# Performance work log

Hardware: AMD Instinct MI355X
Metric: run time of the kernel (lower is better)

Reference implementation:

```python
import jax, jax.numpy as jnp
import numpy as np
import math

HEADS = 8
DIM_KEY = 64
WINDOW = 128
DIM = 512
NUM_REL_POS_FEATURES = 512  # = HEADS*DIM_KEY; %4==0 and %6!=0 -> exp + central_mask features
W_WIDTH, W_FRAC = 8, 4
X_WIDTH, X_FRAC = 8, 4


def quantize(x, width, frac_width):
    # MASE integer_quantizer: fixed-point round+clamp (STE in bwd, identity here).
    scale = 2.0 ** frac_width
    lo = -(2.0 ** (width - 1))
    hi = 2.0 ** (width - 1) - 1.0
    q = jnp.clip(jnp.round(x * scale), lo, hi) / scale
    return x + jax.lax.stop_gradient(q - x)


def get_positional_embed(window, feature_size):
    # distances in [-(W-1), W-1]
    d = jnp.arange(-(window - 1), window, dtype=jnp.float32)  # [2W-1]
    nb = feature_size // 4  # 2 feature fns * 2 components
    ad = jnp.abs(d)[:, None]
    # exponential features
    max_range = math.log(window) / math.log(2.0)
    half_life = 2.0 ** jnp.linspace(3.0, max_range, nb)
    e = jnp.exp(-math.log(2.0) / half_life[None, :] * ad)  # [2W-1, nb]
    # central mask features (2**128 overflows to inf in f32, matching torch)
    cw = 2.0 ** jnp.arange(1, nb + 1, dtype=jnp.float32) - 1.0
    c = (cw[None, :] > ad).astype(jnp.float32)  # [2W-1, nb]
    emb = jnp.concatenate([e, c], axis=-1)  # [2W-1, 2*nb]
    return jnp.concatenate([emb, jnp.sign(d)[:, None] * emb], axis=-1)  # [2W-1, 4*nb]


def relative_shift_swin(x):
    # x: [b, h, w, t1, t2] with t2 = 2*t1 - 1 -> [b, h, w, t1, t1]
    b, h, w, t1, t2 = x.shape
    x = jnp.concatenate([jnp.zeros_like(x[..., :1]), x], axis=-1)  # pad -> t2+1 = 2*t1
    t2p = t2 + 1
    x = x.reshape(b, h, w, t2p, t1)[:, :, :, 1:, :]
    x = x.reshape(b, h, w, t1, t2p - 1)
    return x[..., :(t2p + 1) // 2]


def setup_inputs() -> dict:
    key = jax.random.key(0)
    ks = jax.random.split(key, 7)
    b, n = 4, 8192
    hd = HEADS * DIM_KEY
    return {
        "x": jax.random.normal(ks[0], (b, n, DIM), dtype=jnp.float32),
        "w_qkv": jax.random.normal(ks[1], (hd * 3, DIM), dtype=jnp.float32) * 0.02,
        "w_out": jax.random.normal(ks[2], (DIM, hd), dtype=jnp.float32) * 0.02,
        "b_out": jnp.zeros((DIM,), dtype=jnp.float32),
        "w_rel": jax.random.normal(ks[3], (hd, NUM_REL_POS_FEATURES), dtype=jnp.float32) * 0.02,
        "rel_content_bias": jax.random.normal(ks[4], (1, HEADS, 1, 1, DIM_KEY), dtype=jnp.float32),
        "rel_pos_bias": jax.random.normal(ks[5], (1, HEADS, 1, 1, DIM_KEY), dtype=jnp.float32),
    }


def reference(x, w_qkv, w_out, b_out, w_rel, rel_content_bias, rel_pos_bias):
    b, n, c = x.shape
    w = n // WINDOW  # n divisible by window -> no padding path
    xq = quantize(x, X_WIDTH, X_FRAC)
    wq = quantize(w_qkv, W_WIDTH, W_FRAC)
    wo = quantize(w_out, W_WIDTH, W_FRAC)

    qkv = xq @ wq.T  # [b, n, 3*h*d], last dim laid out as (h, d, k)
    qkv = qkv.reshape(b, n, HEADS, DIM_KEY, 3)
    q = qkv[..., 0].transpose(0, 2, 1, 3)  # [b, h, n, d]
    k = qkv[..., 1].transpose(0, 2, 1, 3)
    v = qkv[..., 2].transpose(0, 2, 1, 3)

    qw = q.reshape(b, HEADS, w, WINDOW, DIM_KEY)
    kw = k.reshape(b, HEADS, w, WINDOW, DIM_KEY)
    vw = v.reshape(b, HEADS, w, WINDOW, DIM_KEY)

    positions = get_positional_embed(WINDOW, NUM_REL_POS_FEATURES)  # [2W-1, F]
    rel_k = positions @ w_rel.T  # [2W-1, h*d]  (rel_pos_embedding weight is NOT quantized)
    rel_k = rel_k.reshape(2 * WINDOW - 1, HEADS, DIM_KEY).transpose(1, 0, 2)  # [h, 2W-1, d]

    scale = DIM_KEY ** -0.5
    content_attn = jnp.einsum('bhwqd,bhwkd->bhwqk', qw + rel_content_bias, kw) * scale
    # NB: positional logits are intentionally unscaled, as in the source.
    rel_logits = jnp.einsum('bhwqd,hkd->bhwqk', qw + rel_pos_bias, rel_k)  # [b,h,w,W,2W-1]
    position_attn = relative_shift_swin(rel_logits)  # [b,h,w,W,W]

    attn = jax.nn.softmax(content_attn + position_attn, axis=-1)
    out = jnp.einsum('bhwqk,bhwkd->bhwqd', attn, vw)  # [b,h,w,W,d]
    out = out.transpose(0, 2, 3, 1, 4).reshape(b, w, WINDOW, HEADS * DIM_KEY)
    out = out @ wo.T + b_out  # [b, w, W, dim]
    return out.reshape(b, n, -1)
```

## Files before the change

kernel.cpp:

```cpp
#include <hip/hip_runtime.h>

typedef unsigned short u16;
typedef unsigned int u32;
typedef __attribute__((ext_vector_type(8))) __bf16 bf16x8;
typedef __attribute__((ext_vector_type(4))) float f32x4;
typedef __attribute__((ext_vector_type(8))) unsigned short u16x8;
typedef __attribute__((ext_vector_type(4))) unsigned short u16x4;

#define GLL(gp, lp) __builtin_amdgcn_global_load_lds((const __attribute__((address_space(1))) void*)(gp), (__attribute__((address_space(3))) void*)(lp), 16, 0, 0)

__device__ __forceinline__ u16 f2bf(float f) {
  u32 u = __float_as_uint(f);
  u += 0x7FFFu + ((u >> 16) & 1u);
  return (u16)(u >> 16);
}
__device__ __forceinline__ float bf2f(u16 u) { return __uint_as_float(((u32)u) << 16); }
__device__ __forceinline__ float qz(float v) {
  float r = rintf(v * 16.0f);
  r = fminf(127.0f, fmaxf(-128.0f, r));
  return r * 0.0625f;
}
__device__ __forceinline__ f32x4 mfma16(bf16x8 a, bf16x8 b, f32x4 c) {
  return __builtin_amdgcn_mfma_f32_16x16x32_bf16(a, b, c, 0, 0, 0);
}

__global__ __launch_bounds__(256) void k_quant(const float* __restrict__ x,
                                               const float* __restrict__ wqkv,
                                               const float* __restrict__ wout,
                                               u16* __restrict__ xq,
                                               u16* __restrict__ wq,
                                               u16* __restrict__ wo) {
  const int X4 = 4194304;
  const int W4 = 196608;
  const int O4 = 65536;
  int stride = gridDim.x * blockDim.x;
  for (int i = blockIdx.x * blockDim.x + threadIdx.x; i < X4 + W4 + O4; i += stride) {
    const float4* s; u16* d; int jl, jd;
    if (i < X4) {
      s = (const float4*)x; d = xq; jl = i; jd = i;
    } else if (i < X4 + W4) {
      s = (const float4*)wqkv; d = wq;
      jl = i - X4;
      int rs = jl >> 7;
      int jc = jl & 127;
      int h = rs / 192;
      int rem = rs - h * 192;
      int dd = rem / 3;
      int comp = rem - dd * 3;
      jd = (comp * 512 + h * 64 + dd) * 128 + jc;
    } else {
      s = (const float4*)wout; d = wo; jl = i - X4 - W4; jd = jl;
    }
    float4 v = s[jl];
    u16x4 o;
    o.x = f2bf(qz(v.x)); o.y = f2bf(qz(v.y)); o.z = f2bf(qz(v.z)); o.w = f2bf(qz(v.w));
    *(u16x4*)(d + (size_t)jd * 4) = o;
  }
}

__global__ __launch_bounds__(128) void k_relk(const float* __restrict__ w_rel,
                                              const float* __restrict__ pb,
                                              u16* __restrict__ relk,
                                              float* __restrict__ pbR) {
  int r = blockIdx.x;
  int cseg = blockIdx.y;
  int tid = threadIdx.x;
  int c = cseg * 128 + tid;
  if (r == 255) {
    relk[((size_t)(c >> 6) * 256 + 255) * 64 + (c & 63)] = 0;
    if ((tid & 63) == 0) pbR[(c >> 6) * 256 + 255] = 0.f;
    return;
  }
  __shared__ float pos[512];
  float dd = (float)(r - 127);
  float ad = fabsf(dd);
  float sg = (dd > 0.f) ? 1.f : ((dd < 0.f) ? -1.f : 0.f);
  for (int f = tid; f < 512; f += 128) {
    int base = f & 255;
    float feat;
    if (base < 128) {
      float hl = exp2f(3.0f + (float)base * (4.0f / 127.0f));
      feat = expf((-0.6931471805599453f / hl) * ad);
    } else {
      float cw = exp2f((float)(base - 128 + 1)) - 1.0f;
      feat = (cw > ad) ? 1.0f : 0.0f;
    }
    if (f >= 256) feat *= sg;
    pos[f] = feat;
  }
  __syncthreads();
  const float4* wr4 = (const float4*)(w_rel + (size_t)c * 512);
  float acc = 0.f;
  #pragma unroll 4
  for (int f4 = 0; f4 < 128; f4++) {
    float4 w4 = wr4[f4];
    int f = f4 * 4;
    acc += pos[f] * w4.x + pos[f + 1] * w4.y + pos[f + 2] * w4.z + pos[f + 3] * w4.w;
  }
  relk[((size_t)(c >> 6) * 256 + r) * 64 + (c & 63)] = f2bf(acc);
  float contrib = acc * pb[c];
  #pragma unroll
  for (int off = 1; off < 64; off <<= 1) contrib += __shfl_xor(contrib, off, 64);
  if ((tid & 63) == 0) pbR[(c >> 6) * 256 + r] = contrib;
}

__global__ __launch_bounds__(256) void k_gemm_qkv(const u16* __restrict__ Aq,
                                                  const u16* __restrict__ Bq,
                                                  u16* __restrict__ Qo,
                                                  u16* __restrict__ Ko,
                                                  u16* __restrict__ Vo) {
  __shared__ u16 As[128 * 32];
  __shared__ u16 Bs[128 * 32];
  int tid = threadIdx.x;
  int bid = blockIdx.x;
  int swz = (bid & 7) * (gridDim.x >> 3) + (bid >> 3);
  int m0 = (swz / 12) * 128, n0 = (swz % 12) * 128;
  int wid = tid >> 6, lane = tid & 63, g = lane >> 4, r16 = lane & 15;
  int wm = wid >> 1, wn = wid & 1;
  f32x4 acc[4][4];
  #pragma unroll
  for (int i = 0; i < 4; i++)
    #pragma unroll
    for (int j = 0; j < 4; j++) acc[i][j] = (f32x4){0.f, 0.f, 0.f, 0.f};
  const u16* Ab = Aq + (size_t)m0 * 512;
  const u16* Bb = Bq + (size_t)n0 * 512;
  char* AsB = (char*)As + wid * 1024;
  char* BsB = (char*)Bs + wid * 1024;
  int srow = tid >> 2;
  int scol = ((tid & 3) ^ ((tid >> 3) & 3)) * 8;
  int gs = (g ^ ((r16 >> 1) & 3)) * 8;
  for (int k0 = 0; k0 < 512; k0 += 32) {
    __syncthreads();
    GLL(Ab + (size_t)srow * 512 + k0 + scol, AsB);
    GLL(Ab + (size_t)(srow + 64) * 512 + k0 + scol, AsB + 4096);
    GLL(Bb + (size_t)srow * 512 + k0 + scol, BsB);
    GLL(Bb + (size_t)(srow + 64) * 512 + k0 + scol, BsB + 4096);
    __syncthreads();
    bf16x8 a[4], b[4];
    #pragma unroll
    for (int mt = 0; mt < 4; mt++)
      a[mt] = *(const bf16x8*)(As + (wm * 64 + mt * 16 + r16) * 32 + gs);
    #pragma unroll
    for (int nt = 0; nt < 4; nt++)
      b[nt] = *(const bf16x8*)(Bs + (wn * 64 + nt * 16 + r16) * 32 + gs);
    #pragma unroll
    for (int mt = 0; mt < 4; mt++)
      #pragma unroll
      for (int nt = 0; nt < 4; nt++) acc[mt][nt] = mfma16(a[mt], b[nt], acc[mt][nt]);
  }
  #pragma unroll
  for (int nt = 0; nt < 4; nt++) {
    int colc = n0 + wn * 64 + nt * 16 + r16;
    int comp = colc >> 9;
    int hd = colc & 511;
    u16* dst = (comp == 0) ? Qo : (comp == 1 ? Ko : Vo);
    u16* dstp = dst + (size_t)(hd >> 6) * 524288 + (hd & 63);
    #pragma unroll
    for (int mt = 0; mt < 4; mt++) {
      int mbase = m0 + wm * 64 + mt * 16 + 4 * g;
      #pragma unroll
      for (int rr = 0; rr < 4; rr++) {
        int m = mbase + rr;
        int bb = m >> 13, nn = m & 8191;
        dstp[(size_t)bb * 4194304 + (size_t)nn * 64] = f2bf(acc[mt][nt][rr]);
      }
    }
  }
}

__global__ __launch_bounds__(512) void k_attn(const u16* __restrict__ Q,
                                              const u16* __restrict__ K,
                                              const u16* __restrict__ V,
                                              const u16* __restrict__ relk,
                                              const float* __restrict__ pbR,
                                              const float* __restrict__ cb,
                                              u16* __restrict__ attout) {
  int bid = blockIdx.x;
  int bb = bid >> 9;
  int h = (bid >> 6) & 7;
  int w = bid & 63;
  int tid = threadIdx.x;
  int s = tid >> 6;
  int lane = tid & 63, g = lane >> 4, r16 = lane & 15;
  const int n0 = w * 128;
  const u16* Qh = Q + ((size_t)(bb * 8 + h) * 8192 + n0) * 64;
  const u16* Kh = K + ((size_t)(bb * 8 + h) * 8192 + n0) * 64;
  const u16* Vh = V + ((size_t)(bb * 8 + h) * 8192 + n0) * 64;
  const u16* Rh = relk + (size_t)h * 256 * 64;
  const float* pbRh = pbR + h * 256;

  __shared__ u16 VT[64 * 128];
  __shared__ u16 Pst[8 * 16 * 128];
  __shared__ float cbK[128];

  {
    int rv = tid >> 2, c0 = (tid & 3) << 4;
    const u16* src = Vh + rv * 64 + c0;
    u16x8 v0 = *(const u16x8*)src;
    u16x8 v1 = *(const u16x8*)(src + 8);
    int chunk = rv >> 3, sub = rv & 7;
    #pragma unroll
    for (int j = 0; j < 8; j++) {
      int dv = c0 + j;
      VT[dv * 128 + ((chunk ^ (dv & 7)) << 3) + sub] = v0[j];
    }
    #pragma unroll
    for (int j = 0; j < 8; j++) {
      int dv = c0 + 8 + j;
      VT[dv * 128 + ((chunk ^ (dv & 7)) << 3) + sub] = v1[j];
    }
  }
  if (tid < 128) {
    const u16x8* kr8 = (const u16x8*)(Kh + tid * 64);
    const float* cbh = cb + h * 64;
    float a = 0.f;
    #pragma unroll
    for (int d8 = 0; d8 < 8; d8++) {
      u16x8 kv = kr8[d8];
      #pragma unroll
      for (int j = 0; j < 8; j++) a += cbh[d8 * 8 + j] * bf2f(kv[j]);
    }
    cbK[tid] = a;
  }

  const u16* qptr = Qh + ((s << 4) + r16) * 64 + (g << 3);
  bf16x8 qa0 = *(const bf16x8*)qptr;
  bf16x8 qa1 = *(const bf16x8*)(qptr + 32);

  f32x4 sc[8];
  #pragma unroll
  for (int kt = 0; kt < 8; kt++) {
    const u16* kp = Kh + ((kt << 4) + r16) * 64 + (g << 3);
    bf16x8 b0 = *(const bf16x8*)kp;
    bf16x8 b1 = *(const bf16x8*)(kp + 32);
    f32x4 c = {0.f, 0.f, 0.f, 0.f};
    c = mfma16(qa0, b0, c);
    sc[kt] = mfma16(qa1, b1, c);
  }
  f32x4 rl[9];
  #pragma unroll
  for (int t = 0; t < 9; t++) {
    int ct = 7 - s + t;
    const u16* rp = Rh + ((ct << 4) + r16) * 64 + (g << 3);
    bf16x8 b0 = *(const bf16x8*)rp;
    bf16x8 b1 = *(const bf16x8*)(rp + 32);
    f32x4 c = {0.f, 0.f, 0.f, 0.f};
    c = mfma16(qa0, b0, c);
    c = mfma16(qa1, b1, c);
    float pv = pbRh[(ct << 4) + r16];
    c[0] += pv; c[1] += pv; c[2] += pv; c[3] += pv;
    rl[t] = c;
  }
  __syncthreads();

  #pragma unroll
  for (int kt = 0; kt < 8; kt++) {
    float cbk = cbK[(kt << 4) + r16];
    #pragma unroll
    for (int rr = 0; rr < 4; rr++) {
      int qq = 4 * g + rr;
      int loc = 15 + r16 - qq;
      int srcl = (g << 4) | (loc & 15);
      float vlo = __shfl(rl[kt][rr], srcl, 64);
      float vhi = __shfl(rl[kt + 1][rr], srcl, 64);
      float pos = (loc < 16) ? vlo : vhi;
      sc[kt][rr] = (sc[kt][rr] + cbk) * 0.125f + pos;
    }
  }
  float inv[4];
  #pragma unroll
  for (int rr = 0; rr < 4; rr++) {
    float m = sc[0][rr];
    #pragma unroll
    for (int kt = 1; kt < 8; kt++) m = fmaxf(m, sc[kt][rr]);
    #pragma unroll
    for (int off = 1; off < 16; off <<= 1) m = fmaxf(m, __shfl_xor(m, off, 64));
    float sum = 0.f;
    #pragma unroll
    for (int kt = 0; kt < 8; kt++) {
      float p = expf(sc[kt][rr] - m);
      sc[kt][rr] = p;
      sum += p;
    }
    #pragma unroll
    for (int off = 1; off < 16; off <<= 1) sum += __shfl_xor(sum, off, 64);
    inv[rr] = 1.0f / sum;
  }
  u16* Pw = Pst + s * (16 * 128);
  #pragma unroll
  for (int kt = 0; kt < 8; kt++) {
    #pragma unroll
    for (int rr = 0; rr < 4; rr++) {
      int qq = 4 * g + rr;
      int k = (kt << 4) + r16;
      Pw[qq * 128 + ((((k >> 3)) ^ (qq & 7)) << 3) + (k & 7)] = f2bf(sc[kt][rr]);
    }
  }
  f32x4 o[4];
  #pragma unroll
  for (int dvt = 0; dvt < 4; dvt++) o[dvt] = (f32x4){0.f, 0.f, 0.f, 0.f};
  #pragma unroll
  for (int koff = 0; koff < 128; koff += 32) {
    int ach = (koff >> 3) + g;
    bf16x8 a = *(const bf16x8*)(Pw + r16 * 128 + ((ach ^ (r16 & 7)) << 3));
    #pragma unroll
    for (int dvt = 0; dvt < 4; dvt++) {
      int dv = dvt * 16 + r16;
      bf16x8 bv = *(const bf16x8*)(VT + dv * 128 + ((ach ^ (dv & 7)) << 3));
      o[dvt] = mfma16(a, bv, o[dvt]);
    }
  }
  #pragma unroll
  for (int dvt = 0; dvt < 4; dvt++) {
    #pragma unroll
    for (int rr = 0; rr < 4; rr++) {
      int qq = 4 * g + rr;
      int nrow = n0 + (s << 4) + qq;
      int colo = h * 64 + dvt * 16 + r16;
      attout[((size_t)bb * 8192 + nrow) * 512 + colo] = f2bf(o[dvt][rr] * inv[rr]);
    }
  }
}

__global__ __launch_bounds__(256) void k_gemm_out(const u16* __restrict__ Aq,
                                                  const u16* __restrict__ Bq,
                                                  const float* __restrict__ bias,
                                                  float* __restrict__ out) {
  __shared__ u16 As[128 * 32];
  __shared__ u16 Bs[128 * 32];
  int tid = threadIdx.x;
  int bid = blockIdx.x;
  int swz = (bid & 7) * (gridDim.x >> 3) + (bid >> 3);
  int m0 = (swz >> 2) * 128, n0 = (swz & 3) * 128;
  int wid = tid >> 6, lane = tid & 63, g = lane >> 4, r16 = lane & 15;
  int wm = wid >> 1, wn = wid & 1;
  f32x4 acc[4][4];
  #pragma unroll
  for (int i = 0; i < 4; i++)
    #pragma unroll
    for (int j = 0; j < 4; j++) acc[i][j] = (f32x4){0.f, 0.f, 0.f, 0.f};
  const u16* Ab = Aq + (size_t)m0 * 512;
  const u16* Bb = Bq + (size_t)n0 * 512;
  char* AsB = (char*)As + wid * 1024;
  char* BsB = (char*)Bs + wid * 1024;
  int srow = tid >> 2;
  int scol = ((tid & 3) ^ ((tid >> 3) & 3)) * 8;
  int gs = (g ^ ((r16 >> 1) & 3)) * 8;
  for (int k0 = 0; k0 < 512; k0 += 32) {
    __syncthreads();
    GLL(Ab + (size_t)srow * 512 + k0 + scol, AsB);
    GLL(Ab + (size_t)(srow + 64) * 512 + k0 + scol, AsB + 4096);
    GLL(Bb + (size_t)srow * 512 + k0 + scol, BsB);
    GLL(Bb + (size_t)(srow + 64) * 512 + k0 + scol, BsB + 4096);
    __syncthreads();
    bf16x8 a[4], b[4];
    #pragma unroll
    for (int mt = 0; mt < 4; mt++)
      a[mt] = *(const bf16x8*)(As + (wm * 64 + mt * 16 + r16) * 32 + gs);
    #pragma unroll
    for (int nt = 0; nt < 4; nt++)
      b[nt] = *(const bf16x8*)(Bs + (wn * 64 + nt * 16 + r16) * 32 + gs);
    #pragma unroll
    for (int mt = 0; mt < 4; mt++)
      #pragma unroll
      for (int nt = 0; nt < 4; nt++) acc[mt][nt] = mfma16(a[mt], b[nt], acc[mt][nt]);
  }
  #pragma unroll
  for (int nt = 0; nt < 4; nt++) {
    int col = n0 + wn * 64 + nt * 16 + r16;
    float bv = bias[col];
    #pragma unroll
    for (int mt = 0; mt < 4; mt++) {
      int mbase = m0 + wm * 64 + mt * 16 + 4 * g;
      #pragma unroll
      for (int rr = 0; rr < 4; rr++) {
        int m = mbase + rr;
        out[(size_t)m * 512 + col] = acc[mt][nt][rr] + bv;
      }
    }
  }
}

extern "C" void kernel_launch(void* const* d_in, const int* in_sizes, int n_in,
                              void* d_out, int out_size, void* d_ws, size_t ws_size,
                              hipStream_t stream) {
  const float* x     = (const float*)d_in[0];
  const float* w_qkv = (const float*)d_in[1];
  const float* w_out = (const float*)d_in[2];
  const float* b_out = (const float*)d_in[3];
  const float* w_rel = (const float*)d_in[4];
  const float* cb    = (const float*)d_in[5];
  const float* pb    = (const float*)d_in[6];
  float* out = (float*)d_out;

  char* p = (char*)d_ws;
  u16* xq   = (u16*)p; p += (size_t)32768 * 512 * 2;
  u16* wq   = (u16*)p; p += (size_t)1536 * 512 * 2;
  u16* wo   = (u16*)p; p += (size_t)512 * 512 * 2;
  u16* relk = (u16*)p; p += (size_t)8 * 256 * 64 * 2;
  float* pbR = (float*)p; p += (size_t)8 * 256 * 4;
  u16* Qb   = (u16*)p; p += (size_t)4 * 8 * 8192 * 64 * 2;
  u16* Kb   = (u16*)p; p += (size_t)4 * 8 * 8192 * 64 * 2;
  u16* Vb   = (u16*)p; p += (size_t)4 * 8 * 8192 * 64 * 2;
  u16* att  = (u16*)p; p += (size_t)32768 * 512 * 2;

  hipLaunchKernelGGL(k_quant, dim3(2048), dim3(256), 0, stream, x, w_qkv, w_out, xq, wq, wo);
  hipLaunchKernelGGL(k_relk, dim3(256, 4), dim3(128), 0, stream, w_rel, pb, relk, pbR);
  hipLaunchKernelGGL(k_gemm_qkv, dim3(3072), dim3(256), 0, stream, xq, wq, Qb, Kb, Vb);
  hipLaunchKernelGGL(k_attn, dim3(2048), dim3(512), 0, stream, Qb, Kb, Vb, relk, pbR, cb, att);
  hipLaunchKernelGGL(k_gemm_out, dim3(1024), dim3(256), 0, stream, att, wo, b_out, out);
}
```

Before: 359.5 us.

## Transpose attention MFMA operands to keep P in registers and drop LDS staging

Swaps the MFMA operand order so each lane owns one query row's scores. The P matrix can then be passed to the PV MFMA through cross-lane shuffles instead of being staged through LDS. Relative-position tiles are now computed inside the score loop and realigned with register rotations plus a single shuffle pair, which lowers register pressure. Softmax reductions need only two xor-shuffles, and outputs are written as packed bf16 pairs. The V transpose uses 32-bit LDS writes, and the launch bounds request higher occupancy, at the cost of extra shuffle work and more intricate lane-index logic.

```diff
diff --git a/kernel.cpp b/kernel.cpp
--- a/kernel.cpp
+++ b/kernel.cpp
@@ -6,6 +6,7 @@
 typedef __attribute__((ext_vector_type(4))) float f32x4;
 typedef __attribute__((ext_vector_type(8))) unsigned short u16x8;
 typedef __attribute__((ext_vector_type(4))) unsigned short u16x4;
+typedef __attribute__((ext_vector_type(4))) unsigned int u32x4;
 
 #define GLL(gp, lp) __builtin_amdgcn_global_load_lds((const __attribute__((address_space(1))) void*)(gp), (__attribute__((address_space(3))) void*)(lp), 16, 0, 0)
 
@@ -15,6 +16,11 @@
   return (u16)(u >> 16);
 }
 __device__ __forceinline__ float bf2f(u16 u) { return __uint_as_float(((u32)u) << 16); }
+__device__ __forceinline__ u32 cvtpk(float lo, float hi) {
+  u32 r;
+  asm("v_cvt_pk_bf16_f32 %0, %1, %2" : "=v"(r) : "v"(lo), "v"(hi));
+  return r;
+}
 __device__ __forceinline__ float qz(float v) {
   float r = rintf(v * 16.0f);
   r = fminf(127.0f, fmaxf(-128.0f, r));
@@ -168,13 +174,28 @@
   }
 }
 
-__global__ __launch_bounds__(512) void k_attn(const u16* __restrict__ Q,
-                                              const u16* __restrict__ K,
-                                              const u16* __restrict__ V,
-                                              const u16* __restrict__ relk,
-                                              const float* __restrict__ pbR,
-                                              const float* __restrict__ cb,
-                                              u16* __restrict__ attout) {
+__device__ __forceinline__ f32x4 rel_tile(const u16* __restrict__ Rh,
+                                          const float* __restrict__ pbRh,
+                                          bf16x8 qb0, bf16x8 qb1,
+                                          int ct, int r16, int g) {
+  const u16* rp = Rh + ((ct << 4) + r16) * 64 + (g << 3);
+  bf16x8 rb0 = *(const bf16x8*)rp;
+  bf16x8 rb1 = *(const bf16x8*)(rp + 32);
+  f32x4 c = {0.f, 0.f, 0.f, 0.f};
+  c = mfma16(rb0, qb0, c);
+  c = mfma16(rb1, qb1, c);
+  f32x4 pv = *(const f32x4*)(pbRh + (ct << 4) + (g << 2));
+  c[0] += pv[0]; c[1] += pv[1]; c[2] += pv[2]; c[3] += pv[3];
+  return c;
+}
+
+__global__ __launch_bounds__(512, 8) void k_attn(const u16* __restrict__ Q,
+                                                 const u16* __restrict__ K,
+                                                 const u16* __restrict__ V,
+                                                 const u16* __restrict__ relk,
+                                                 const float* __restrict__ pbR,
+                                                 const float* __restrict__ cb,
+                                                 u16* __restrict__ attout) {
   int bid = blockIdx.x;
   int bb = bid >> 9;
   int h = (bid >> 6) & 7;
@@ -190,24 +211,22 @@
   const float* pbRh = pbR + h * 256;
 
   __shared__ u16 VT[64 * 128];
-  __shared__ u16 Pst[8 * 16 * 128];
   __shared__ float cbK[128];
 
   {
-    int rv = tid >> 2, c0 = (tid & 3) << 4;
-    const u16* src = Vh + rv * 64 + c0;
+    int r2 = tid >> 3;
+    int c0 = (tid & 7) << 3;
+    const u16* src = Vh + r2 * 128 + c0;
     u16x8 v0 = *(const u16x8*)src;
-    u16x8 v1 = *(const u16x8*)(src + 8);
-    int chunk = rv >> 3, sub = rv & 7;
+    u16x8 v1 = *(const u16x8*)(src + 64);
+    int kc = r2 >> 2;
+    int pos = (r2 & 3) << 1;
     #pragma unroll
     for (int j = 0; j < 8; j++) {
       int dv = c0 + j;
-      VT[dv * 128 + ((chunk ^ (dv & 7)) << 3) + sub] = v0[j];
-    }
-    #pragma unroll
-    for (int j = 0; j < 8; j++) {
-      int dv = c0 + 8 + j;
-      VT[dv * 128 + ((chunk ^ (dv & 7)) << 3) + sub] = v1[j];
+      int swzv = (dv ^ (dv >> 3)) & 7;
+      u32 wv = (u32)v0[j] | ((u32)v1[j] << 16);
+      *(u32*)(VT + dv * 128 + ((kc ^ swzv) << 3) + pos) = wv;
     }
   }
   if (tid < 128) {
@@ -224,100 +243,124 @@
   }
 
   const u16* qptr = Qh + ((s << 4) + r16) * 64 + (g << 3);
-  bf16x8 qa0 = *(const bf16x8*)qptr;
-  bf16x8 qa1 = *(const bf16x8*)(qptr + 32);
+  bf16x8 qb0 = *(const bf16x8*)qptr;
+  bf16x8 qb1 = *(const bf16x8*)(qptr + 32);
 
   f32x4 sc[8];
   #pragma unroll
   for (int kt = 0; kt < 8; kt++) {
     const u16* kp = Kh + ((kt << 4) + r16) * 64 + (g << 3);
-    bf16x8 b0 = *(const bf16x8*)kp;
-    bf16x8 b1 = *(const bf16x8*)(kp + 32);
+    bf16x8 kf0 = *(const bf16x8*)kp;
+    bf16x8 kf1 = *(const bf16x8*)(kp + 32);
     f32x4 c = {0.f, 0.f, 0.f, 0.f};
-    c = mfma16(qa0, b0, c);
-    sc[kt] = mfma16(qa1, b1, c);
-  }
-  f32x4 rl[9];
-  #pragma unroll
-  for (int t = 0; t < 9; t++) {
-    int ct = 7 - s + t;
-    const u16* rp = Rh + ((ct << 4) + r16) * 64 + (g << 3);
-    bf16x8 b0 = *(const bf16x8*)rp;
-    bf16x8 b1 = *(const bf16x8*)(rp + 32);
-    f32x4 c = {0.f, 0.f, 0.f, 0.f};
-    c = mfma16(qa0, b0, c);
-    c = mfma16(qa1, b1, c);
-    float pv = pbRh[(ct << 4) + r16];
-    c[0] += pv; c[1] += pv; c[2] += pv; c[3] += pv;
-    rl[t] = c;
-  }
+    c = mfma16(kf0, qb0, c);
+    sc[kt] = mfma16(kf1, qb1, c);
+  }
+
+  int a0 = (3 - r16) & 3;
+  bool rb0s = (a0 & 1) != 0, rb1s = (a0 & 2) != 0;
+  float rotA[4], rotB[4];
+  {
+    f32x4 rl = rel_tile(Rh, pbRh, qb0, qb1, 7 - s, r16, g);
+    float s1[4];
+    #pragma unroll
+    for (int i = 0; i < 4; i++) s1[i] = rb0s ? rl[(i + 1) & 3] : rl[i];
+    #pragma unroll
+    for (int i = 0; i < 4; i++) rotA[i] = rb1s ? s1[(i + 2) & 3] : s1[i];
+  }
+  int srcl[4]; bool hisel[4];
+  #pragma unroll
+  for (int rr = 0; rr < 4; rr++) {
+    int loc = 15 + 4 * g + rr - r16;
+    srcl[rr] = (((loc & 15) >> 2) << 4) | r16;
+    hisel[rr] = loc >= 16;
+  }
+
   __syncthreads();
 
   #pragma unroll
   for (int kt = 0; kt < 8; kt++) {
-    float cbk = cbK[(kt << 4) + r16];
+    f32x4 rl = rel_tile(Rh, pbRh, qb0, qb1, 8 - s + kt, r16, g);
+    float s1[4];
+    #pragma unroll
+    for (int i = 0; i < 4; i++) s1[i] = rb0s ? rl[(i + 1) & 3] : rl[i];
+    #pragma unroll
+    for (int i = 0; i < 4; i++) rotB[i] = rb1s ? s1[(i + 2) & 3] : s1[i];
+    f32x4 cbv = *(const f32x4*)(&cbK[(kt << 4) + (g << 2)]);
     #pragma unroll
     for (int rr = 0; rr < 4; rr++) {
-      int qq = 4 * g + rr;
-      int loc = 15 + r16 - qq;
-      int srcl = (g << 4) | (loc & 15);
-      float vlo = __shfl(rl[kt][rr], srcl, 64);
-      float vhi = __shfl(rl[kt + 1][rr], srcl, 64);
-      float pos = (loc < 16) ? vlo : vhi;
-      sc[kt][rr] = (sc[kt][rr] + cbk) * 0.125f + pos;
-    }
-  }
-  float inv[4];
-  #pragma unroll
-  for (int rr = 0; rr < 4; rr++) {
-    float m = sc[0][rr];
-    #pragma unroll
-    for (int kt = 1; kt < 8; kt++) m = fmaxf(m, sc[kt][rr]);
-    #pragma unroll
-    for (int off = 1; off < 16; off <<= 1) m = fmaxf(m, __shfl_xor(m, off, 64));
-    float sum = 0.f;
-    #pragma unroll
-    for (int kt = 0; kt < 8; kt++) {
-      float p = expf(sc[kt][rr] - m);
+      float vlo = __shfl(rotA[rr], srcl[rr], 64);
+      float vhi = __shfl(rotB[rr], srcl[rr], 64);
+      float posv = hisel[rr] ? vhi : vlo;
+      sc[kt][rr] = (sc[kt][rr] + cbv[rr]) * 0.125f + posv;
+    }
+    #pragma unroll
+    for (int i = 0; i < 4; i++) rotA[i] = rotB[i];
+  }
+
+  float mx = sc[0][0];
+  #pragma unroll
+  for (int kt = 0; kt < 8; kt++)
+    #pragma unroll
+    for (int rr = 0; rr < 4; rr++) mx = fmaxf(mx, sc[kt][rr]);
+  mx = fmaxf(mx, __shfl_xor(mx, 16, 64));
+  mx = fmaxf(mx, __shfl_xor(mx, 32, 64));
+  float sum = 0.f;
+  #pragma unroll
+  for (int kt = 0; kt < 8; kt++)
+    #pragma unroll
+    for (int rr = 0; rr < 4; rr++) {
+      float p = expf(sc[kt][rr] - mx);
       sc[kt][rr] = p;
       sum += p;
     }
-    #pragma unroll
-    for (int off = 1; off < 16; off <<= 1) sum += __shfl_xor(sum, off, 64);
-    inv[rr] = 1.0f / sum;
-  }
-  u16* Pw = Pst + s * (16 * 128);
+  sum += __shfl_xor(sum, 16, 64);
+  sum += __shfl_xor(sum, 32, 64);
+  float inv = 1.0f / sum;
+
+  u32 pkb[8][2];
   #pragma unroll
   for (int kt = 0; kt < 8; kt++) {
-    #pragma unroll
-    for (int rr = 0; rr < 4; rr++) {
-      int qq = 4 * g + rr;
-      int k = (kt << 4) + r16;
-      Pw[qq * 128 + ((((k >> 3)) ^ (qq & 7)) << 3) + (k & 7)] = f2bf(sc[kt][rr]);
-    }
-  }
+    pkb[kt][0] = cvtpk(sc[kt][0], sc[kt][1]);
+    pkb[kt][1] = cvtpk(sc[kt][2], sc[kt][3]);
+  }
+
   f32x4 o[4];
   #pragma unroll
   for (int dvt = 0; dvt < 4; dvt++) o[dvt] = (f32x4){0.f, 0.f, 0.f, 0.f};
-  #pragma unroll
-  for (int koff = 0; koff < 128; koff += 32) {
-    int ach = (koff >> 3) + g;
-    bf16x8 a = *(const bf16x8*)(Pw + r16 * 128 + ((ach ^ (r16 & 7)) << 3));
+  int L0 = ((g & 1) << 5) | r16;
+  int L1 = L0 + 16;
+  bool ghi = g >= 2;
+  #pragma unroll
+  for (int ks = 0; ks < 4; ks++) {
+    int e = 2 * ks;
+    u32 w0a = __shfl((int)pkb[e][0], L0, 64), w0b = __shfl((int)pkb[e + 1][0], L0, 64);
+    u32 w1a = __shfl((int)pkb[e][1], L0, 64), w1b = __shfl((int)pkb[e + 1][1], L0, 64);
+    u32 w2a = __shfl((int)pkb[e][0], L1, 64), w2b = __shfl((int)pkb[e + 1][0], L1, 64);
+    u32 w3a = __shfl((int)pkb[e][1], L1, 64), w3b = __shfl((int)pkb[e + 1][1], L1, 64);
+    u32x4 wv;
+    wv.x = ghi ? w0b : w0a;
+    wv.y = ghi ? w1b : w1a;
+    wv.z = ghi ? w2b : w2a;
+    wv.w = ghi ? w3b : w3a;
+    bf16x8 pf = __builtin_bit_cast(bf16x8, wv);
     #pragma unroll
     for (int dvt = 0; dvt < 4; dvt++) {
-      int dv = dvt * 16 + r16;
-      bf16x8 bv = *(const bf16x8*)(VT + dv * 128 + ((ach ^ (dv & 7)) << 3));
-      o[dvt] = mfma16(a, bv, o[dvt]);
-    }
-  }
+      int dv = (dvt << 4) | r16;
+      int swzv = (dv ^ (dv >> 3)) & 7;
+      bf16x8 vf = *(const bf16x8*)(VT + dv * 128 + (((ks * 4 + g) ^ swzv) << 3));
+      o[dvt] = mfma16(vf, pf, o[dvt]);
+    }
+  }
+
+  int nrow = n0 + (s << 4) + r16;
+  u16* orow = attout + ((size_t)bb * 8192 + nrow) * 512 + h * 64;
   #pragma unroll
   for (int dvt = 0; dvt < 4; dvt++) {
     #pragma unroll
-    for (int rr = 0; rr < 4; rr++) {
-      int qq = 4 * g + rr;
-      int nrow = n0 + (s << 4) + qq;
-      int colo = h * 64 + dvt * 16 + r16;
-      attout[((size_t)bb * 8192 + nrow) * 512 + colo] = f2bf(o[dvt][rr] * inv[rr]);
+    for (int pr = 0; pr < 2; pr++) {
+      u32 wv = cvtpk(o[dvt][2 * pr] * inv, o[dvt][2 * pr + 1] * inv);
+      *(u32*)(orow + (dvt << 4) + (g << 2) + (pr << 1)) = wv;
     }
   }
 }
```

New measurement: 440.4 us. +22.5%, slower.
